# Performance work log

Measured on AMD Instinct MI355X. Metric: run time of the kernel, lower is better.

Reference implementation:

```python
import jax, jax.numpy as jnp
import numpy as np

NBATCH, NATOM, NEIGH = 16, 512, 64
NTYPE, NWAVE, NIPSIN, NORBIT = 4, 8, 3, 128
CUTOFF = 5.0
NPAIR = NATOM * NEIGH  # neighbor pairs per configuration


def _make_index_para(nipsin):
    # [0, 1,1,1, 2,...(9 times)] -> angular-order label per channel
    parts = [np.zeros(1, np.int32)]
    for i in range(1, nipsin):
        parts.append(np.full(3 ** i, i, np.int32))
    return jnp.asarray(np.concatenate(parts))


def setup_inputs() -> dict:
    key = jax.random.key(0)
    ks = jax.random.split(key, 10)
    cart = jax.random.uniform(ks[0], (NBATCH, NATOM, 3), jnp.float32) * 6.0
    numatoms = jnp.full((NBATCH,), NATOM, dtype=jnp.int32)
    species = jax.random.randint(ks[1], (NBATCH * NATOM,), 0, NTYPE).astype(jnp.int32)
    atom_index = jax.random.randint(ks[2], (2, NBATCH, NPAIR), 0, NATOM).astype(jnp.int32)
    shifts = jnp.zeros((NBATCH, NPAIR, 3), jnp.float32)  # all pairs valid (pass >-1e10 check)
    # learned parameters / buffers
    rs = jnp.tile(jnp.linspace(0.5, 4.0, NWAVE, dtype=jnp.float32)[None, :], (NTYPE, 1))
    inta = -(jax.random.uniform(ks[3], (NTYPE, NWAVE), jnp.float32) * 0.9 + 0.1)
    params = jnp.ones((NTYPE, NWAVE), jnp.float32) / float(NEIGH)
    hyper = jax.random.normal(ks[4], (1, NIPSIN, NWAVE, NORBIT), jnp.float32) * (1.0 / np.sqrt(NWAVE))
    index_para = _make_index_para(NIPSIN)
    return {"cart": cart, "numatoms": numatoms, "species": species,
            "atom_index": atom_index, "shifts": shifts,
            "rs": rs, "inta": inta, "params": params, "hyper": hyper,
            "index_para": index_para, "cutoff": CUTOFF}


def _angular(dist_vec, f_cut, nipsin):
    # dist_vec: [N,3], f_cut: [N] -> [L, N] with L = 1 + 3 + ... + 3^(nipsin-1)
    dv = dist_vec.T  # [3, N]
    orb = f_cut[None, :]
    parts = [orb]
    for _ in range(1, nipsin):
        orb = (orb[:, None, :] * dv[None, :, :]).reshape(-1, dv.shape[1])
        parts.append(orb)
    return jnp.concatenate(parts, axis=0)


def reference(cart, numatoms, species, atom_index, shifts, rs, inta, params, hyper, index_para, cutoff):
    nbatch, natom, _ = cart.shape
    totnatom = nbatch * natom
    cart_ = cart.reshape(totnatom, 3)
    # offset per-config neighbor indices to global atom ids
    offs = (jnp.arange(nbatch, dtype=atom_index.dtype) * natom)[None, :, None]
    idx12 = (atom_index + offs).reshape(2, -1)  # [2, Npairs]
    dist_vec = cart_[idx12[0]] - cart_[idx12[1]] + shifts.reshape(-1, 3)  # [Npairs,3]
    distances = jnp.linalg.norm(dist_vec, axis=-1)  # [Npairs]
    sp_j = species[idx12[1]]
    f_cut = jnp.square(0.5 * jnp.cos(distances * (jnp.pi / cutoff)) + 0.5)
    # per-pair gaussian radial basis, gathered by neighbor element type
    radial = jnp.exp(inta[sp_j] * jnp.square(distances[:, None] - rs[sp_j]))  # [Npairs, nwave]
    ang = _angular(dist_vec, f_cut, NIPSIN)  # [L, Npairs]
    orbital = ang.T[:, :, None] * radial[:, None, :]  # [Npairs, L, nwave]
    orb_coeff = params[species]  # [totnatom, nwave] (all species >= 0)
    # iteration 0 (ocmod_list is empty, so no refinement loop)
    worb = orbital * orb_coeff[idx12[1]][:, None, :]  # [Npairs, L, nwave]
    sum_worb = jax.ops.segment_sum(worb, idx12[0], num_segments=totnatom)  # [totnatom, L, nwave]
    hp = hyper[0][index_para]  # [L, nwave, norbit]
    hw = jnp.einsum('ijk,jkm->ijm', sum_worb, hp)  # [totnatom, L, norbit]
    density = jnp.sum(jnp.square(hw), axis=1)  # [totnatom, norbit]
    return density
```

## Files before the change

### kernel.cpp

```cpp
#include <hip/hip_runtime.h>
#include <hip/hip_bf16.h>

#define NBATCH  16
#define NATOM   512
#define NEIGH   64
#define NPAIR   (NATOM * NEIGH)
#define TOTPAIR (NBATCH * NPAIR)
#define TOTATOM (NBATCH * NATOM)
#define NTYPE   4
#define NWAVE   8
#define NL      13
#define NORBIT  128
#define CAP     128
#define CAPP    130
#define NSUB    8
#define SUBCAP  40
#define PAIRS_PER_SUB (NPAIR / NSUB)


__global__ __launch_bounds__(512) void fill_kernel(
    const int* __restrict__ atom_index,
    int*       __restrict__ count,
    unsigned short* __restrict__ bucket)
{
    const int b   = blockIdx.x >> 3;
    const int s   = blockIdx.x & 7;
    const int tid = threadIdx.x;

    __shared__ int s_cnt[NATOM];
    s_cnt[tid] = 0;
    __syncthreads();

#pragma unroll
    for (int it = 0; it < PAIRS_PER_SUB / 512; ++it) {
        int pl = s * PAIRS_PER_SUB + it * 512 + tid;
        int il = atom_index[b * NPAIR + pl];
        int slot = atomicAdd(&s_cnt[il], 1);
        if (slot < SUBCAP)
            bucket[((size_t)((b * NATOM + il) * NSUB + s)) * SUBCAP + slot] =
                (unsigned short)pl;
    }
    __syncthreads();

    count[(b * NATOM + tid) * NSUB + s] = s_cnt[tid];
}

__global__ __launch_bounds__(128) void gather_kernel(
    const float* __restrict__ cart,
    const int*   __restrict__ species,
    const int*   __restrict__ atom_index,
    const float* __restrict__ shifts,
    const float* __restrict__ rs,
    const float* __restrict__ inta,
    const float* __restrict__ params,
    const float* __restrict__ cutoff_p,
    const int*   __restrict__ count,
    const unsigned short* __restrict__ bucket,
    const float* __restrict__ hyper,
    float*       __restrict__ out)
{
    const int i    = blockIdx.x;
    const int b    = i >> 9;
    const int base = b << 9;
    const int tid  = threadIdx.x;

    __shared__ float s_a [NL][CAPP];
    __shared__ float s_rp[NWAVE][CAPP];
    __shared__ float s_S [NL * NWAVE];
    __shared__ float s_tab[3 * NTYPE * NWAVE];
    __shared__ int   s_off[NSUB + 1];

    if (tid < NTYPE * NWAVE) {
        s_tab[tid]                     = rs[tid];
        s_tab[NTYPE * NWAVE + tid]     = inta[tid];
        s_tab[2 * NTYPE * NWAVE + tid] = params[tid];
    }
    if (tid == 0) {
        int o = 0;
#pragma unroll
        for (int s2 = 0; s2 < NSUB; ++s2) {
            s_off[s2] = o;
            int c = count[i * NSUB + s2];
            o += (c < SUBCAP ? c : SUBCAP);
        }
        s_off[NSUB] = o;
    }
    __syncthreads();

    int total = s_off[NSUB];
    if (total > CAP) total = CAP;

    const float cx  = cart[3 * i + 0];
    const float cy  = cart[3 * i + 1];
    const float cz  = cart[3 * i + 2];
    const float pic = 3.14159265358979323846f / cutoff_p[0];

    for (int k = tid; k < total; k += 128) {
        int s2 = 0;
#pragma unroll
        for (int t = 1; t < NSUB; ++t)
            if (k >= s_off[t]) s2 = t;
        int local = k - s_off[s2];
        int pl = (int)bucket[((size_t)(i * NSUB + s2)) * SUBCAP + local];
        int p  = (b << 15) | pl;
        int j  = atom_index[TOTPAIR + p] + base;

        float dx = cx - cart[3 * j + 0] + shifts[3 * p + 0];
        float dy = cy - cart[3 * j + 1] + shifts[3 * p + 1];
        float dz = cz - cart[3 * j + 2] + shifts[3 * p + 2];
        float d  = sqrtf(dx * dx + dy * dy + dz * dz);

        float c  = 0.5f * __cosf(d * pic) + 0.5f;
        float fc = c * c;

        float a1 = fc * dx, a2 = fc * dy, a3 = fc * dz;
        s_a[0][k]  = fc;
        s_a[1][k]  = a1;       s_a[2][k]  = a2;       s_a[3][k]  = a3;
        s_a[4][k]  = a1 * dx;  s_a[5][k]  = a1 * dy;  s_a[6][k]  = a1 * dz;
        s_a[7][k]  = a2 * dx;  s_a[8][k]  = a2 * dy;  s_a[9][k]  = a2 * dz;
        s_a[10][k] = a3 * dx;  s_a[11][k] = a3 * dy;  s_a[12][k] = a3 * dz;

        int sp = species[j];
#pragma unroll
        for (int w = 0; w < NWAVE; ++w) {
            float tt = d - s_tab[sp * NWAVE + w];
            s_rp[w][k] = __expf(s_tab[NTYPE * NWAVE + sp * NWAVE + w] * tt * tt)
                       * s_tab[2 * NTYPE * NWAVE + sp * NWAVE + w];
        }
    }
    __syncthreads();

    if (tid < NL * NWAVE) {
        int l = tid >> 3, w = tid & 7;
        float S = 0.0f;
        int k = 0;
        for (; k + 1 < total; k += 2) {
            float2 av = *(const float2*)&s_a[l][k];
            float2 rv = *(const float2*)&s_rp[w][k];
            S += av.x * rv.x;
            S += av.y * rv.y;
        }
        if (k < total) S += s_a[l][k] * s_rp[w][k];
        s_S[tid] = S;
    }
    __syncthreads();

    const int m = tid;
    float acc = 0.0f;
#pragma unroll
    for (int l = 0; l < NL; ++l) {
        int ip = (l == 0) ? 0 : ((l < 4) ? 1 : 2);
        const float* hp = hyper + (size_t)ip * (NWAVE * NORBIT) + m;
        float h = 0.0f;
#pragma unroll
        for (int w = 0; w < NWAVE; ++w)
            h += s_S[l * NWAVE + w] * hp[w * NORBIT];
        acc += h * h;
    }
    out[(size_t)i * NORBIT + m] = acc;
}

extern "C" void kernel_launch(void* const* d_in, const int* in_sizes, int n_in,
                              void* d_out, int out_size, void* d_ws, size_t ws_size,
                              hipStream_t stream) {
    const float* cart       = (const float*)d_in[0];
    const int*   species    = (const int*)  d_in[2];
    const int*   atom_index = (const int*)  d_in[3];
    const float* shifts     = (const float*)d_in[4];
    const float* rs         = (const float*)d_in[5];
    const float* inta       = (const float*)d_in[6];
    const float* params     = (const float*)d_in[7];
    const float* hyper      = (const float*)d_in[8];
    const float* cutoff_p   = (const float*)d_in[10];

    int* count = (int*)d_ws;
    unsigned short* bucket =
        (unsigned short*)((char*)d_ws + (size_t)TOTATOM * NSUB * sizeof(int));
    float* out = (float*)d_out;

    fill_kernel<<<NBATCH * NSUB, 512, 0, stream>>>(atom_index, count, bucket);

    gather_kernel<<<TOTATOM, 128, 0, stream>>>(
        cart, species, atom_index, shifts, rs, inta, params, cutoff_p,
        count, bucket, hyper, out);
}
```

Baseline: 107.9 us.

## Use bf16 MFMA with hi/lo split for per-atom contractions

Replaces the scalar pair-sum reduction and the hyper projection with bf16 MFMA 16x16x32 instructions. The radial and hyper values are split into hi and lo bf16 parts to keep some precision. A new small kernel pre-packs hyper into MFMA fragment layout in the workspace. This removes scalar FMA loops and repeated global hyper reads per block, at the cost of an extra launch, bf16 rounding of the angular and intermediate terms, and a single wave doing the first contraction.

```diff
diff --git a/kernel.cpp b/kernel.cpp
--- a/kernel.cpp
+++ b/kernel.cpp
@@ -12,11 +12,45 @@
 #define NL      13
 #define NORBIT  128
 #define CAP     128
-#define CAPP    130
 #define NSUB    8
 #define SUBCAP  40
 #define PAIRS_PER_SUB (NPAIR / NSUB)
 
+#define AST     136
+#define S2ST    40
+
+#define WS_HFRAG_OFF 5505024
+
+typedef __attribute__((ext_vector_type(8))) short  short8;
+typedef __attribute__((ext_vector_type(4))) float  f32x4;
+
+static __device__ inline unsigned short f2bf(float f) {
+    unsigned u = __builtin_bit_cast(unsigned, f);
+    u += 0x7FFFu + ((u >> 16) & 1u);
+    return (unsigned short)(u >> 16);
+}
+static __device__ inline float bf2f(unsigned short h) {
+    unsigned u = ((unsigned)h) << 16;
+    return __builtin_bit_cast(float, u);
+}
+
+__global__ void hfrag_kernel(const float* __restrict__ hyper,
+                             unsigned short* __restrict__ hfrag) {
+    const int s    = blockIdx.x >> 3;
+    const int n    = blockIdx.x & 7;
+    const int lane = threadIdx.x;
+    const int q    = lane >> 4;
+    const int col  = n * 16 + (lane & 15);
+#pragma unroll
+    for (int j = 0; j < 8; ++j) {
+        int k = q * 8 + j;
+        float f = (k < 24) ? hyper[(k >> 3) * (NWAVE * NORBIT) + (k & 7) * NORBIT + col]
+                           : 0.0f;
+        unsigned short hi = f2bf(f);
+        unsigned short v  = (s == 0) ? hi : f2bf(f - bf2f(hi));
+        hfrag[((size_t)(blockIdx.x * 64 + lane)) * 8 + j] = v;
+    }
+}
 
 __global__ __launch_bounds__(512) void fill_kernel(
     const int* __restrict__ atom_index,
@@ -56,52 +90,67 @@
     const float* __restrict__ cutoff_p,
     const int*   __restrict__ count,
     const unsigned short* __restrict__ bucket,
-    const float* __restrict__ hyper,
+    const unsigned short* __restrict__ hfrag,
     float*       __restrict__ out)
 {
-    const int i    = blockIdx.x;
-    const int b    = i >> 9;
-    const int base = b << 9;
-    const int tid  = threadIdx.x;
-
-    __shared__ float s_a [NL][CAPP];
-    __shared__ float s_rp[NWAVE][CAPP];
-    __shared__ float s_S [NL * NWAVE];
+    const int i      = blockIdx.x;
+    const int b      = i >> 9;
+    const int base   = b << 9;
+    const int tid    = threadIdx.x;
+    const int lane   = tid & 63;
+    const int waveId = tid >> 6;
+
+    __shared__ __attribute__((aligned(16))) unsigned short s_A[16 * AST];
+    __shared__ __attribute__((aligned(16))) unsigned short s_B[24 * AST];
+    __shared__ __attribute__((aligned(16))) unsigned short s_S2[16 * S2ST];
     __shared__ float s_tab[3 * NTYPE * NWAVE];
+    __shared__ int   s_cv[NSUB];
     __shared__ int   s_off[NSUB + 1];
+
+    short8 hb[4], lb[4];
+#pragma unroll
+    for (int t = 0; t < 4; ++t) {
+        int n = waveId * 4 + t;
+        hb[t] = *(const short8*)&hfrag[((size_t)(n * 64 + lane)) * 8];
+        lb[t] = *(const short8*)&hfrag[((size_t)((8 + n) * 64 + lane)) * 8];
+    }
 
     if (tid < NTYPE * NWAVE) {
         s_tab[tid]                     = rs[tid];
         s_tab[NTYPE * NWAVE + tid]     = inta[tid];
         s_tab[2 * NTYPE * NWAVE + tid] = params[tid];
     }
+    if (tid >= 64 && tid < 64 + NSUB) {
+        int c = count[i * NSUB + (tid - 64)];
+        s_cv[tid - 64] = c < SUBCAP ? c : SUBCAP;
+    }
+    for (int e = tid; e < 16 * S2ST; e += 128) s_S2[e] = 0;
+    __syncthreads();
+
     if (tid == 0) {
         int o = 0;
 #pragma unroll
-        for (int s2 = 0; s2 < NSUB; ++s2) {
-            s_off[s2] = o;
-            int c = count[i * NSUB + s2];
-            o += (c < SUBCAP ? c : SUBCAP);
-        }
+        for (int s2 = 0; s2 < NSUB; ++s2) { s_off[s2] = o; o += s_cv[s2]; }
         s_off[NSUB] = o;
     }
     __syncthreads();
 
     int total = s_off[NSUB];
     if (total > CAP) total = CAP;
+    const int T = (total + 31) >> 5;
 
     const float cx  = cart[3 * i + 0];
     const float cy  = cart[3 * i + 1];
     const float cz  = cart[3 * i + 2];
     const float pic = 3.14159265358979323846f / cutoff_p[0];
 
-    for (int k = tid; k < total; k += 128) {
+    if (tid < total) {
+        const int k = tid;
         int s2 = 0;
 #pragma unroll
         for (int t = 1; t < NSUB; ++t)
             if (k >= s_off[t]) s2 = t;
-        int local = k - s_off[s2];
-        int pl = (int)bucket[((size_t)(i * NSUB + s2)) * SUBCAP + local];
+        int pl = (int)bucket[((size_t)(i * NSUB + s2)) * SUBCAP + (k - s_off[s2])];
         int p  = (b << 15) | pl;
         int j  = atom_index[TOTPAIR + p] + base;
 
@@ -114,50 +163,79 @@
         float fc = c * c;
 
         float a1 = fc * dx, a2 = fc * dy, a3 = fc * dz;
-        s_a[0][k]  = fc;
-        s_a[1][k]  = a1;       s_a[2][k]  = a2;       s_a[3][k]  = a3;
-        s_a[4][k]  = a1 * dx;  s_a[5][k]  = a1 * dy;  s_a[6][k]  = a1 * dz;
-        s_a[7][k]  = a2 * dx;  s_a[8][k]  = a2 * dy;  s_a[9][k]  = a2 * dz;
-        s_a[10][k] = a3 * dx;  s_a[11][k] = a3 * dy;  s_a[12][k] = a3 * dz;
+        s_A[0 * AST + k]  = f2bf(fc);
+        s_A[1 * AST + k]  = f2bf(a1);      s_A[2 * AST + k]  = f2bf(a2);
+        s_A[3 * AST + k]  = f2bf(a3);
+        s_A[4 * AST + k]  = f2bf(a1 * dx); s_A[5 * AST + k]  = f2bf(a1 * dy);
+        s_A[6 * AST + k]  = f2bf(a1 * dz);
+        s_A[7 * AST + k]  = f2bf(a2 * dx); s_A[8 * AST + k]  = f2bf(a2 * dy);
+        s_A[9 * AST + k]  = f2bf(a2 * dz);
+        s_A[10 * AST + k] = f2bf(a3 * dx); s_A[11 * AST + k] = f2bf(a3 * dy);
+        s_A[12 * AST + k] = f2bf(a3 * dz);
 
         int sp = species[j];
 #pragma unroll
         for (int w = 0; w < NWAVE; ++w) {
             float tt = d - s_tab[sp * NWAVE + w];
-            s_rp[w][k] = __expf(s_tab[NTYPE * NWAVE + sp * NWAVE + w] * tt * tt)
-                       * s_tab[2 * NTYPE * NWAVE + sp * NWAVE + w];
-        }
-    }
-    __syncthreads();
-
-    if (tid < NL * NWAVE) {
-        int l = tid >> 3, w = tid & 7;
-        float S = 0.0f;
-        int k = 0;
-        for (; k + 1 < total; k += 2) {
-            float2 av = *(const float2*)&s_a[l][k];
-            float2 rv = *(const float2*)&s_rp[w][k];
-            S += av.x * rv.x;
-            S += av.y * rv.y;
-        }
-        if (k < total) S += s_a[l][k] * s_rp[w][k];
-        s_S[tid] = S;
-    }
-    __syncthreads();
-
-    const int m = tid;
-    float acc = 0.0f;
-#pragma unroll
-    for (int l = 0; l < NL; ++l) {
-        int ip = (l == 0) ? 0 : ((l < 4) ? 1 : 2);
-        const float* hp = hyper + (size_t)ip * (NWAVE * NORBIT) + m;
-        float h = 0.0f;
-#pragma unroll
-        for (int w = 0; w < NWAVE; ++w)
-            h += s_S[l * NWAVE + w] * hp[w * NORBIT];
-        acc += h * h;
-    }
-    out[(size_t)i * NORBIT + m] = acc;
+            float rp = __expf(s_tab[NTYPE * NWAVE + sp * NWAVE + w] * tt * tt)
+                     * s_tab[2 * NTYPE * NWAVE + sp * NWAVE + w];
+            unsigned short hi = f2bf(rp);
+            s_B[w * AST + k]       = hi;
+            s_B[(8 + w) * AST + k] = f2bf(rp - bf2f(hi));
+        }
+    }
+    if (T > 0 && total < T * 32) {
+        int tb = (T - 1) << 5;
+        for (int e = tid; e < 16 * 32; e += 128) {
+            int row = e >> 5, k = tb + (e & 31);
+            if (k >= total) { s_A[row * AST + k] = 0; s_B[row * AST + k] = 0; }
+        }
+    }
+    __syncthreads();
+
+    if (waveId == 0) {
+        const int m = lane & 15, q = lane >> 4;
+        f32x4 acc = {0.f, 0.f, 0.f, 0.f};
+        for (int t = 0; t < T; ++t) {
+            short8 af  = *(const short8*)&s_A[m * AST + t * 32 + q * 8];
+            short8 bhf = *(const short8*)&s_B[m * AST + t * 32 + q * 8];
+            short8 blf = *(const short8*)&s_B[(m + 8) * AST + t * 32 + q * 8];
+            acc = __builtin_amdgcn_mfma_f32_16x16x32_bf16(af, bhf, acc, 0, 0, 0);
+            acc = __builtin_amdgcn_mfma_f32_16x16x32_bf16(af, blf, acc, 0, 0, 0);
+        }
+        if (m < 8) {
+#pragma unroll
+            for (int reg = 0; reg < 4; ++reg) {
+                int l = q * 4 + reg;
+                if (l < 13) {
+                    int ip = (l == 0) ? 0 : ((l < 4) ? 1 : 2);
+                    s_S2[l * S2ST + ip * 8 + m] = f2bf(acc[reg]);
+                }
+            }
+        }
+    }
+    __syncthreads();
+
+    {
+        const int m = lane & 15, q = lane >> 4;
+        short8 sf = *(const short8*)&s_S2[m * S2ST + q * 8];
+#pragma unroll
+        for (int t = 0; t < 4; ++t) {
+            f32x4 acc = {0.f, 0.f, 0.f, 0.f};
+            acc = __builtin_amdgcn_mfma_f32_16x16x32_bf16(sf, hb[t], acc, 0, 0, 0);
+            acc = __builtin_amdgcn_mfma_f32_16x16x32_bf16(sf, lb[t], acc, 0, 0, 0);
+            float part = 0.f;
+#pragma unroll
+            for (int reg = 0; reg < 4; ++reg) {
+                int l = q * 4 + reg;
+                if (l < 13) part += acc[reg] * acc[reg];
+            }
+            part += __shfl_xor(part, 16);
+            part += __shfl_xor(part, 32);
+            if (lane < 16)
+                out[(size_t)i * NORBIT + (waveId * 4 + t) * 16 + lane] = part;
+        }
+    }
 }
 
 extern "C" void kernel_launch(void* const* d_in, const int* in_sizes, int n_in,
@@ -176,11 +254,14 @@
     int* count = (int*)d_ws;
     unsigned short* bucket =
         (unsigned short*)((char*)d_ws + (size_t)TOTATOM * NSUB * sizeof(int));
+    unsigned short* hfrag = (unsigned short*)((char*)d_ws + WS_HFRAG_OFF);
     float* out = (float*)d_out;
+
+    hfrag_kernel<<<16, 64, 0, stream>>>(hyper, hfrag);
 
     fill_kernel<<<NBATCH * NSUB, 512, 0, stream>>>(atom_index, count, bucket);
 
     gather_kernel<<<TOTATOM, 128, 0, stream>>>(
         cart, species, atom_index, shifts, rs, inta, params, cutoff_p,
-        count, bucket, hyper, out);
-}
+        count, bucket, hfrag, out);
+}
```

Result: slower. 111.5 us (+3.4%).
